# Kernel tuning notes

Hardware: AMD Instinct MI355X
Metric: run time of the kernel (lower is better)

Reference implementation:

```python
import jax, jax.numpy as jnp
import numpy as np

WS, SS, NH = 7, 3, 16  # window_size, shift_size, num_heads


def _rel_pos_index(ws):
    coords = np.stack(np.meshgrid(np.arange(ws), np.arange(ws), indexing='ij'))  # (2, ws, ws)
    cf = coords.reshape(2, -1)                       # (2, N)
    rel = (cf[:, :, None] - cf[:, None, :]).transpose(1, 2, 0).copy()  # (N, N, 2)
    rel[:, :, 0] += ws - 1
    rel[:, :, 1] += ws - 1
    rel[:, :, 0] *= 2 * ws - 1
    return rel.sum(-1)                               # (N, N) int indices into bias table


def _attn_mask(Hp, Wp, ws, ss):
    img = np.zeros((Hp, Wp))
    slices = (slice(0, -ws), slice(-ws, -ss), slice(-ss, None))
    cnt = 0
    for h in slices:
        for w in slices:
            img[h, w] = cnt
            cnt += 1
    mw = img.reshape(Hp // ws, ws, Wp // ws, ws).transpose(0, 2, 1, 3).reshape(-1, ws * ws)  # (nW, N)
    am = mw[:, None, :] - mw[:, :, None]             # (nW, N, N)
    return np.where(am != 0, -100.0, 0.0).astype(np.float32)


def setup_inputs() -> dict:
    key = jax.random.key(0)
    k1, k2, k3, k4 = jax.random.split(key, 4)
    B, H, W, C = 16, 56, 56, 512
    return {
        'q_out': jax.random.normal(k1, (B, H, W, C), dtype=jnp.float32),
        'k_out': jax.random.normal(k2, (B, H, W, C), dtype=jnp.float32),
        'v_out': jax.random.normal(k3, (B, H, W, C), dtype=jnp.float32),
        'bias_table': 0.02 * jax.random.normal(k4, ((2 * WS - 1) ** 2, NH), dtype=jnp.float32),
        'C': C, 'H': H, 'W': W,
        'x_low_padding_h': 0, 'x_low_padding_w': 0,
    }


def reference(q_out, k_out, v_out, bias_table, C, H, W, x_low_padding_h, x_low_padding_w):
    ws, ss, nh = WS, SS, NH
    Hp, Wp = H + x_low_padding_h, W + x_low_padding_w
    B = q_out.shape[0]
    hd = C // nh
    scale = hd ** (-0.5)
    N = ws * ws

    def part(x):  # (B,Hp,Wp,C) -> (B*nW, N, C)
        x = x.reshape(B, Hp // ws, ws, Wp // ws, ws, C).transpose(0, 1, 3, 2, 4, 5)
        return x.reshape(-1, N, C)

    # cyclic shift
    sq = jnp.roll(q_out, (-ss, -ss), axis=(1, 2))
    sk = jnp.roll(k_out, (-ss, -ss), axis=(1, 2))
    sv = jnp.roll(v_out, (-ss, -ss), axis=(1, 2))

    qw, kw, vw = part(sq), part(sk), part(sv)
    B_ = qw.shape[0]
    q = qw.reshape(B_, N, nh, hd).transpose(0, 2, 1, 3) * scale  # (B_, nh, N, hd)
    k = kw.reshape(B_, N, nh, hd).transpose(0, 2, 1, 3)
    v = vw.reshape(B_, N, nh, hd).transpose(0, 2, 1, 3)

    attn = jnp.einsum('bhnd,bhmd->bhnm', q, k)  # (B_, nh, N, N)

    # relative position bias
    rpi = _rel_pos_index(ws)
    bias = bias_table[rpi.reshape(-1)].reshape(N, N, nh).transpose(2, 0, 1)  # (nh, N, N)
    attn = attn + bias[None]

    # shift mask
    am = jnp.asarray(_attn_mask(Hp, Wp, ws, ss), dtype=attn.dtype)  # (nW, N, N)
    nW = am.shape[0]
    attn = attn.reshape(B_ // nW, nW, nh, N, N) + am[None, :, None]
    attn = jax.nn.softmax(attn.reshape(B_, nh, N, N), axis=-1)

    xw = jnp.einsum('bhnm,bhmd->bhnd', attn, v).transpose(0, 2, 1, 3).reshape(B_, N, C)

    # window reverse + reverse shift
    x = xw.reshape(B, Hp // ws, Wp // ws, ws, ws, C).transpose(0, 1, 3, 2, 4, 5).reshape(B, Hp, Wp, C)
    return jnp.roll(x, (ss, ss), axis=(1, 2))
```

## Files before the change

kernel.cpp:

```cpp
#include <hip/hip_runtime.h>
#include <stdint.h>


constexpr int WSZ  = 7;
constexpr int NTOK = 49;
constexpr int NH_  = 16;
constexpr int HD_  = 32;
constexpr int SP   = 56;
constexpr int CH   = 512;
constexpr float LOG2E = 1.4426950408889634f;

typedef float    f32x4 __attribute__((ext_vector_type(4)));
typedef short    s16x8 __attribute__((ext_vector_type(8)));
typedef _Float16 f16x4 __attribute__((ext_vector_type(4)));

union FragU { uint32_t w[4]; s16x8 v; };

__device__ __forceinline__ uint32_t bf16_hibits(float x) {
    uint32_t u = __float_as_uint(x);
    u += 0x7fffu + ((u >> 16) & 1u);
    return u & 0xffff0000u;
}
__device__ __forceinline__ uint32_t pk_bf16(float a, float b) {
    return (bf16_hibits(a) >> 16) | bf16_hibits(b);
}

__global__ __launch_bounds__(256)
void build_bm(const float* __restrict__ bias, _Float16* __restrict__ bm)
{
    const int blk = blockIdx.x;
    const int h = blk >> 2, cls = blk & 3;
    for (int idx = threadIdx.x; idx < 4096; idx += 256) {
        const int q = idx >> 6, m = idx & 63;
        float val;
        if (q >= NTOK || m >= NTOK) {
            val = -1000.0f;
        } else {
            const int iq = q / 7, jq = q % 7, im = m / 7, jm = m % 7;
            const int rpi = (iq - im + 6) * 13 + (jq - jm + 6);
            const float bv = bias[rpi * NH_ + h];
            const int rq = ((cls & 2) ? (iq < 4 ? 3 : 6) : 0)
                         + ((cls & 1) ? (jq < 4 ? 1 : 2) : 0);
            const int rm = ((cls & 2) ? (im < 4 ? 3 : 6) : 0)
                         + ((cls & 1) ? (jm < 4 ? 1 : 2) : 0);
            const float mask = (rq != rm) ? -100.0f : 0.0f;
            val = (bv + mask) * LOG2E;
        }
        bm[blk * 4096 + idx] = (_Float16)val;
    }
}

struct Raw {
    float4 q[4][2];
    float4 k[4][2];
    float  v[2][2][8];
};
struct Frag {
    s16x8 Qh[4], Kh[4], Vb[2][2];
};

__device__ __forceinline__ int make_off(int wh, int lane) {
    const int h  = wh & 15;
    const int w  = wh >> 4;
    const int wc = w & 7, wr = (w >> 3) & 7, b = w >> 6;
    const int t  = lane < NTOK ? lane : NTOK - 1;
    const int it = t / 7, jt = t - 7 * it;
    int sr = wr * 7 + it + 3; if (sr >= SP) sr -= SP;
    int sc = wc * 7 + jt + 3; if (sc >= SP) sc -= SP;
    return ((b * SP + sr) * SP + sc) * CH + h * HD_;
}
__device__ __forceinline__ int cls_of(int wh) {
    const int w = wh >> 4;
    return ((((w >> 3) & 7) == 7) ? 2 : 0) | (((w & 7) == 7) ? 1 : 0);
}

__device__ __forceinline__ void issue_qkv(const float* __restrict__ qg,
                                          const float* __restrict__ kg,
                                          const float* __restrict__ vg,
                                          int off, int l16, int g, Raw& r,
                                          int (&oQK)[4]) {
#pragma unroll
    for (int tt = 0; tt < 4; ++tt) oQK[tt] = __shfl(off, 16 * tt + l16);
    int oV[16];
#pragma unroll
    for (int mc = 0; mc < 2; ++mc)
#pragma unroll
        for (int e = 0; e < 8; ++e) oV[8 * mc + e] = __shfl(off, 32 * mc + 8 * g + e);
#pragma unroll
    for (int tt = 0; tt < 4; ++tt) {
        const float* qp = qg + oQK[tt] + 8 * g;
        const float* kp = kg + oQK[tt] + 8 * g;
        r.q[tt][0] = *(const float4*)qp;  r.q[tt][1] = *(const float4*)(qp + 4);
        r.k[tt][0] = *(const float4*)kp;  r.k[tt][1] = *(const float4*)(kp + 4);
    }
#pragma unroll
    for (int mc = 0; mc < 2; ++mc)
#pragma unroll
        for (int dh = 0; dh < 2; ++dh)
#pragma unroll
            for (int e = 0; e < 8; ++e)
                r.v[mc][dh][e] = vg[oV[8 * mc + e] + 16 * dh + l16];
}

__device__ __forceinline__ void convertQKV(const Raw& r, float qs, Frag& f) {
#pragma unroll
    for (int tt = 0; tt < 4; ++tt) {
        FragU qh, kh;
        qh.w[0] = pk_bf16(r.q[tt][0].x * qs, r.q[tt][0].y * qs);
        qh.w[1] = pk_bf16(r.q[tt][0].z * qs, r.q[tt][0].w * qs);
        qh.w[2] = pk_bf16(r.q[tt][1].x * qs, r.q[tt][1].y * qs);
        qh.w[3] = pk_bf16(r.q[tt][1].z * qs, r.q[tt][1].w * qs);
        kh.w[0] = pk_bf16(r.k[tt][0].x, r.k[tt][0].y);
        kh.w[1] = pk_bf16(r.k[tt][0].z, r.k[tt][0].w);
        kh.w[2] = pk_bf16(r.k[tt][1].x, r.k[tt][1].y);
        kh.w[3] = pk_bf16(r.k[tt][1].z, r.k[tt][1].w);
        f.Qh[tt] = qh.v; f.Kh[tt] = kh.v;
    }
#pragma unroll
    for (int mc = 0; mc < 2; ++mc)
#pragma unroll
        for (int dh = 0; dh < 2; ++dh) {
            FragU fu;
#pragma unroll
            for (int wd = 0; wd < 4; ++wd)
                fu.w[wd] = pk_bf16(r.v[mc][dh][2 * wd], r.v[mc][dh][2 * wd + 1]);
            f.Vb[mc][dh] = fu.v;
        }
}

__device__ __forceinline__ void load_bm(const _Float16* __restrict__ bmh,
                                        int l16, int g, f16x4 (&bmr)[4][4]) {
#pragma unroll
    for (int tq = 0; tq < 4; ++tq)
#pragma unroll
        for (int tk = 0; tk < 4; ++tk)
            bmr[tq][tk] = *(const f16x4*)(bmh + (16 * tq + l16) * 64 + 16 * tk + 4 * g);
}

__device__ __forceinline__ void do_math(const Frag& f, const f16x4 (&bmr)[4][4],
                                        const int (&oQK)[4], int lane, int g, int l16,
                                        float* __restrict__ outg) {
    uint32_t u0[4][4], u1[4][4];
    float inv[4];
#pragma unroll
    for (int tq = 0; tq < 4; ++tq) {
        float dsum = 0.f;
#pragma unroll
        for (int tk = 0; tk < 4; ++tk) {
            f32x4 a;
            a[0] = (float)bmr[tq][tk][0] - 23.f;
            a[1] = (float)bmr[tq][tk][1] - 23.f;
            a[2] = (float)bmr[tq][tk][2] - 23.f;
            a[3] = (float)bmr[tq][tk][3] - 23.f;
            a = __builtin_amdgcn_mfma_f32_16x16x32_bf16(f.Kh[tk], f.Qh[tq], a, 0, 0, 0);
            float e0 = __builtin_amdgcn_exp2f(a[0]);
            float e1 = __builtin_amdgcn_exp2f(a[1]);
            float e2 = __builtin_amdgcn_exp2f(a[2]);
            float e3 = __builtin_amdgcn_exp2f(a[3]);
            dsum += (e0 + e1) + (e2 + e3);
            u0[tq][tk] = pk_bf16(e0, e1);
            u1[tq][tk] = pk_bf16(e2, e3);
        }
        dsum += __shfl_xor(dsum, 16);
        dsum += __shfl_xor(dsum, 32);
        inv[tq] = 1.0f / (dsum + 1e-30f);
    }

    const int srcb = 32 * (g & 1) + l16;
    const bool hiG = (lane >= 32);
    s16x8 PA[4][2];
#pragma unroll
    for (int tq = 0; tq < 4; ++tq)
#pragma unroll
        for (int mc = 0; mc < 2; ++mc) {
            FragU fu;
#pragma unroll
            for (int wd = 0; wd < 4; ++wd) {
                const int sl = srcb + 16 * (wd >> 1);
                uint32_t A, B;
                if (wd & 1) {
                    A = __shfl(u1[tq][2 * mc],     sl);
                    B = __shfl(u1[tq][2 * mc + 1], sl);
                } else {
                    A = __shfl(u0[tq][2 * mc],     sl);
                    B = __shfl(u0[tq][2 * mc + 1], sl);
                }
                fu.w[wd] = hiG ? B : A;
            }
            PA[tq][mc] = fu.v;
        }

#pragma unroll
    for (int tq = 0; tq < 4; ++tq) {
        const float iv = inv[tq];
        const bool ok = (tq < 3) || (l16 == 0);
#pragma unroll
        for (int dh = 0; dh < 2; ++dh) {
            f32x4 a = {0.f, 0.f, 0.f, 0.f};
            a = __builtin_amdgcn_mfma_f32_16x16x32_bf16(f.Vb[0][dh], PA[tq][0], a, 0, 0, 0);
            a = __builtin_amdgcn_mfma_f32_16x16x32_bf16(f.Vb[1][dh], PA[tq][1], a, 0, 0, 0);
            if (ok) {
                float4 st;
                st.x = a[0] * iv; st.y = a[1] * iv;
                st.z = a[2] * iv; st.w = a[3] * iv;
                *(float4*)(outg + oQK[tq] + 16 * dh + 4 * g) = st;
            }
        }
    }
}

__global__ __launch_bounds__(256, 2)
void swin_pipe_kernel(const float* __restrict__ qg,
                      const float* __restrict__ kg,
                      const float* __restrict__ vg,
                      const _Float16* __restrict__ bm,
                      float* __restrict__ outg)
{
    const int wave = threadIdx.x >> 6;
    const int gw   = blockIdx.x * 4 + wave;
    const int lane = threadIdx.x & 63;
    const int g    = lane >> 4;
    const int l16  = lane & 15;
    const float qs = 0.17677669529663687f * LOG2E;

    const int h = gw & 15;
    const _Float16* bmhead = bm + (size_t)h * 4 * 4096;

    Raw A, B;
    Frag f;
    f16x4 bmr[4][4];
    int oA[4], oB[4];

    const int wh0 = gw;
    const int off0 = make_off(wh0, lane);
    issue_qkv(qg, kg, vg, off0, l16, g, A, oA);

    convertQKV(A, qs, f);
    load_bm(bmhead + cls_of(wh0) * 4096, l16, g, bmr);
    const int wh1 = gw + 4096;
    const int off1 = make_off(wh1, lane);
    issue_qkv(qg, kg, vg, off1, l16, g, B, oB);
    __builtin_amdgcn_sched_barrier(0);
    do_math(f, bmr, oA, lane, g, l16, outg);

    convertQKV(B, qs, f);
    load_bm(bmhead + cls_of(wh1) * 4096, l16, g, bmr);
    const int wh2 = gw + 8192;
    const int off2 = make_off(wh2, lane);
    issue_qkv(qg, kg, vg, off2, l16, g, A, oA);
    __builtin_amdgcn_sched_barrier(0);
    do_math(f, bmr, oB, lane, g, l16, outg);

    convertQKV(A, qs, f);
    load_bm(bmhead + cls_of(wh2) * 4096, l16, g, bmr);
    const int wh3 = gw + 12288;
    const int off3 = make_off(wh3, lane);
    issue_qkv(qg, kg, vg, off3, l16, g, B, oB);
    __builtin_amdgcn_sched_barrier(0);
    do_math(f, bmr, oA, lane, g, l16, outg);

    convertQKV(B, qs, f);
    load_bm(bmhead + cls_of(wh3) * 4096, l16, g, bmr);
    __builtin_amdgcn_sched_barrier(0);
    do_math(f, bmr, oB, lane, g, l16, outg);
}

__global__ __launch_bounds__(256)
void swin_block_scalar(const float* __restrict__ qg,
                       const float* __restrict__ kg,
                       const float* __restrict__ vg,
                       const float* __restrict__ bias,
                       float* __restrict__ outg)
{
    const int wave = __builtin_amdgcn_readfirstlane(threadIdx.x >> 6);
    const int wh   = blockIdx.x * 4 + wave;
    const int h    = wh & (NH_ - 1);
    const int w    = wh >> 4;
    const int wc   = w & 7;
    const int wr   = (w >> 3) & 7;
    const int b    = w >> 6;

    const int lane = threadIdx.x & 63;
    const int rr   = lane < NTOK ? lane : NTOK - 1;
    const int i    = rr / WSZ;
    const int j    = rr - i * WSZ;

    const int hp = wr * WSZ + i;
    const int wp = wc * WSZ + j;
    int sr = hp + 3; if (sr >= SP) sr -= SP;
    int sc = wp + 3; if (sc >= SP) sc -= SP;
    const int rowoff = ((b * SP + sr) * SP + sc) * CH + h * HD_;
    const int reg_r = (hp < 49 ? 0 : (hp < 53 ? 3 : 6))
                    + (wp < 49 ? 0 : (wp < 53 ? 1 : 2));
    const float qscale = 0.17677669529663687f * LOG2E;

    float qr[HD_];
    {
        const float4* qp = reinterpret_cast<const float4*>(qg + rowoff);
#pragma unroll
        for (int tt = 0; tt < HD_ / 4; ++tt) {
            float4 x = qp[tt];
            qr[4*tt+0] = x.x * qscale; qr[4*tt+1] = x.y * qscale;
            qr[4*tt+2] = x.z * qscale; qr[4*tt+3] = x.w * qscale;
        }
    }
    const int biaslane = (i * 13 + j) * 16 + h;
    float o[HD_];
#pragma unroll
    for (int d = 0; d < HD_; ++d) o[d] = 0.f;
    float denom = 0.f;
    const float* kb = kg + b * SP * SP * CH + h * HD_;
    const float* vb = vg + b * SP * SP * CH + h * HD_;

    for (int ic = 0; ic < WSZ; ++ic) {
        const int hpc = wr * WSZ + ic;
        int src_r = hpc + 3; if (src_r >= SP) src_r -= SP;
        const int regh_c = (hpc < 49 ? 0 : (hpc < 53 ? 3 : 6));
        const float* krow0 = kb + src_r * SP * CH;
        const float* vrow0 = vb + src_r * SP * CH;
        float e[WSZ];
#pragma unroll
        for (int u = 0; u < WSZ; ++u) {
            const int wpc = wc * WSZ + u;
            int src_c = wpc + 3; if (src_c >= SP) src_c -= SP;
            const int reg_c = regh_c + (wpc < 49 ? 0 : (wpc < 53 ? 1 : 2));
            const float* krow = krow0 + src_c * CH;
            const float bv = bias[biaslane + ((6 - ic) * 13 + (6 - u)) * 16];
            float s0 = fmaf(bv, LOG2E, (reg_r != reg_c) ? -167.26950408889634f : -23.0f);
            float s1 = 0.f, s2 = 0.f, s3 = 0.f;
#pragma unroll
            for (int d = 0; d < HD_; d += 4) {
                s0 = fmaf(qr[d+0], krow[d+0], s0);
                s1 = fmaf(qr[d+1], krow[d+1], s1);
                s2 = fmaf(qr[d+2], krow[d+2], s2);
                s3 = fmaf(qr[d+3], krow[d+3], s3);
            }
            e[u] = exp2f((s0 + s1) + (s2 + s3));
            denom += e[u];
        }
#pragma unroll
        for (int u = 0; u < WSZ; ++u) {
            const int wpc = wc * WSZ + u;
            int src_c = wpc + 3; if (src_c >= SP) src_c -= SP;
            const float* vrow = vrow0 + src_c * CH;
            const float ev = e[u];
#pragma unroll
            for (int d = 0; d < HD_; ++d) o[d] = fmaf(ev, vrow[d], o[d]);
        }
    }
    const float invd = 1.0f / denom;
    if (lane < NTOK) {
        float4* op = reinterpret_cast<float4*>(outg + rowoff);
#pragma unroll
        for (int tt = 0; tt < HD_ / 4; ++tt) {
            float4 x;
            x.x = o[4*tt+0] * invd; x.y = o[4*tt+1] * invd;
            x.z = o[4*tt+2] * invd; x.w = o[4*tt+3] * invd;
            op[tt] = x;
        }
    }
}

extern "C" void kernel_launch(void* const* d_in, const int* in_sizes, int n_in,
                              void* d_out, int out_size, void* d_ws, size_t ws_size,
                              hipStream_t stream) {
    const float* q    = (const float*)d_in[0];
    const float* k    = (const float*)d_in[1];
    const float* v    = (const float*)d_in[2];
    const float* bias = (const float*)d_in[3];
    float* out        = (float*)d_out;

    const int B   = in_sizes[0] / (SP * SP * CH);
    const int nwh = B * (SP / WSZ) * (SP / WSZ) * NH_;

    const size_t bm_bytes = (size_t)NH_ * 4 * 4096 * sizeof(_Float16);
    if (ws_size >= bm_bytes) {
        _Float16* bm = (_Float16*)d_ws;
        hipLaunchKernelGGL(build_bm, dim3(NH_ * 4), dim3(256), 0, stream, bias, bm);
        hipLaunchKernelGGL(swin_pipe_kernel, dim3(nwh / 16), dim3(256), 0, stream,
                           q, k, v, bm, out);
    } else {
        hipLaunchKernelGGL(swin_block_scalar, dim3(nwh / 4), dim3(256), 0, stream,
                           q, k, v, bias, out);
    }
}
```

Before: 111.3 us.

## Stream K through LDS via global_load_lds and shorten per-wave pipeline depth

K tiles are now loaded straight into a per-wave LDS slot with global_load_lds instead of into registers, which frees VGPRs. Launch bounds rise from 2 to 3 blocks per CU and each wave handles 2 windows instead of 4, with twice as many blocks. The aim is more waves in flight to hide memory latency. In exchange, each wave overlaps loads with compute over fewer windows, adds explicit vmcnt/lgkmcnt waits, and reuses one LDS slot, so the first window's K must be fully read out of LDS before the second load overwrites it.

```diff
diff --git a/kernel.cpp b/kernel.cpp
--- a/kernel.cpp
+++ b/kernel.cpp
@@ -10,6 +10,9 @@
 constexpr int CH   = 512;
 constexpr float LOG2E = 1.4426950408889634f;
 
+constexpr int SLOT_BYTES = 8192;
+constexpr size_t LDS_BYTES = 4 * SLOT_BYTES;
+
 typedef float    f32x4 __attribute__((ext_vector_type(4)));
 typedef short    s16x8 __attribute__((ext_vector_type(8)));
 typedef _Float16 f16x4 __attribute__((ext_vector_type(4)));
@@ -23,6 +26,13 @@
 }
 __device__ __forceinline__ uint32_t pk_bf16(float a, float b) {
     return (bf16_hibits(a) >> 16) | bf16_hibits(b);
+}
+
+__device__ __forceinline__ void glds16(const float* g, void* l) {
+    __builtin_amdgcn_global_load_lds(
+        (const __attribute__((address_space(1))) uint32_t*)g,
+        (__attribute__((address_space(3))) uint32_t*)l,
+        16, 0, 0);
 }
 
 __global__ __launch_bounds__(256)
@@ -50,14 +60,8 @@
     }
 }
 
-struct Raw {
-    float4 q[4][2];
-    float4 k[4][2];
-    float  v[2][2][8];
-};
-struct Frag {
-    s16x8 Qh[4], Kh[4], Vb[2][2];
-};
+struct QV { float4 q[4][2]; float v[2][2][8]; };
+struct Frag { s16x8 Qh[4], Kh[4], Vb[2][2]; };
 
 __device__ __forceinline__ int make_off(int wh, int lane) {
     const int h  = wh & 15;
@@ -74,11 +78,21 @@
     return ((((w >> 3) & 7) == 7) ? 2 : 0) | (((w & 7) == 7) ? 1 : 0);
 }
 
-__device__ __forceinline__ void issue_qkv(const float* __restrict__ qg,
-                                          const float* __restrict__ kg,
-                                          const float* __restrict__ vg,
-                                          int off, int l16, int g, Raw& r,
-                                          int (&oQK)[4]) {
+__device__ __forceinline__ void glds_K(const float* __restrict__ kg,
+                                       int off, int l16, int g, char* slot) {
+#pragma unroll
+    for (int tt = 0; tt < 4; ++tt) {
+        const int o = __shfl(off, 16 * tt + l16);
+        const float* kp = kg + o + 8 * g;
+        glds16(kp,     slot + (tt * 2 + 0) * 1024);
+        glds16(kp + 4, slot + (tt * 2 + 1) * 1024);
+    }
+}
+
+__device__ __forceinline__ void issue_qv(const float* __restrict__ qg,
+                                         const float* __restrict__ vg,
+                                         int off, int l16, int g, QV& r,
+                                         int (&oQK)[4]) {
 #pragma unroll
     for (int tt = 0; tt < 4; ++tt) oQK[tt] = __shfl(off, 16 * tt + l16);
     int oV[16];
@@ -89,9 +103,7 @@
 #pragma unroll
     for (int tt = 0; tt < 4; ++tt) {
         const float* qp = qg + oQK[tt] + 8 * g;
-        const float* kp = kg + oQK[tt] + 8 * g;
         r.q[tt][0] = *(const float4*)qp;  r.q[tt][1] = *(const float4*)(qp + 4);
-        r.k[tt][0] = *(const float4*)kp;  r.k[tt][1] = *(const float4*)(kp + 4);
     }
 #pragma unroll
     for (int mc = 0; mc < 2; ++mc)
@@ -102,18 +114,21 @@
                 r.v[mc][dh][e] = vg[oV[8 * mc + e] + 16 * dh + l16];
 }
 
-__device__ __forceinline__ void convertQKV(const Raw& r, float qs, Frag& f) {
+__device__ __forceinline__ void convert_all(const char* slot, const QV& r,
+                                            float qs, int lane, Frag& f) {
 #pragma unroll
     for (int tt = 0; tt < 4; ++tt) {
+        const float4 k0 = *(const float4*)(slot + (tt * 2 + 0) * 1024 + lane * 16);
+        const float4 k1 = *(const float4*)(slot + (tt * 2 + 1) * 1024 + lane * 16);
         FragU qh, kh;
         qh.w[0] = pk_bf16(r.q[tt][0].x * qs, r.q[tt][0].y * qs);
         qh.w[1] = pk_bf16(r.q[tt][0].z * qs, r.q[tt][0].w * qs);
         qh.w[2] = pk_bf16(r.q[tt][1].x * qs, r.q[tt][1].y * qs);
         qh.w[3] = pk_bf16(r.q[tt][1].z * qs, r.q[tt][1].w * qs);
-        kh.w[0] = pk_bf16(r.k[tt][0].x, r.k[tt][0].y);
-        kh.w[1] = pk_bf16(r.k[tt][0].z, r.k[tt][0].w);
-        kh.w[2] = pk_bf16(r.k[tt][1].x, r.k[tt][1].y);
-        kh.w[3] = pk_bf16(r.k[tt][1].z, r.k[tt][1].w);
+        kh.w[0] = pk_bf16(k0.x, k0.y);
+        kh.w[1] = pk_bf16(k0.z, k0.w);
+        kh.w[2] = pk_bf16(k1.x, k1.y);
+        kh.w[3] = pk_bf16(k1.z, k1.w);
         f.Qh[tt] = qh.v; f.Kh[tt] = kh.v;
     }
 #pragma unroll
@@ -209,14 +224,25 @@
     }
 }
 
-__global__ __launch_bounds__(256, 2)
-void swin_pipe_kernel(const float* __restrict__ qg,
-                      const float* __restrict__ kg,
-                      const float* __restrict__ vg,
-                      const _Float16* __restrict__ bm,
-                      float* __restrict__ outg)
+__device__ __forceinline__ void wait_vmem() {
+    asm volatile("s_waitcnt vmcnt(0)" ::: "memory");
+    __builtin_amdgcn_sched_barrier(0);
+}
+__device__ __forceinline__ void drain_lds() {
+    asm volatile("s_waitcnt lgkmcnt(0)" ::: "memory");
+    __builtin_amdgcn_sched_barrier(0);
+}
+
+__global__ __launch_bounds__(256, 3)
+void swin_d2_kernel(const float* __restrict__ qg,
+                    const float* __restrict__ kg,
+                    const float* __restrict__ vg,
+                    const _Float16* __restrict__ bm,
+                    float* __restrict__ outg)
 {
+    extern __shared__ char smem[];
     const int wave = threadIdx.x >> 6;
+    char* slot = smem + wave * SLOT_BYTES;
     const int gw   = blockIdx.x * 4 + wave;
     const int lane = threadIdx.x & 63;
     const int g    = lane >> 4;
@@ -226,43 +252,31 @@
     const int h = gw & 15;
     const _Float16* bmhead = bm + (size_t)h * 4 * 4096;
 
-    Raw A, B;
+    const int wh0 = gw, wh1 = gw + 8192;
+    QV r0, r1;
     Frag f;
     f16x4 bmr[4][4];
-    int oA[4], oB[4];
-
-    const int wh0 = gw;
+    int oQK0[4], oQK1[4];
+
     const int off0 = make_off(wh0, lane);
-    issue_qkv(qg, kg, vg, off0, l16, g, A, oA);
-
-    convertQKV(A, qs, f);
+    glds_K(kg, off0, l16, g, slot);
+    issue_qv(qg, vg, off0, l16, g, r0, oQK0);
+
+    wait_vmem();
+    convert_all(slot, r0, qs, lane, f);
+    drain_lds();
+    const int off1 = make_off(wh1, lane);
+    glds_K(kg, off1, l16, g, slot);
+    issue_qv(qg, vg, off1, l16, g, r1, oQK1);
     load_bm(bmhead + cls_of(wh0) * 4096, l16, g, bmr);
-    const int wh1 = gw + 4096;
-    const int off1 = make_off(wh1, lane);
-    issue_qkv(qg, kg, vg, off1, l16, g, B, oB);
     __builtin_amdgcn_sched_barrier(0);
-    do_math(f, bmr, oA, lane, g, l16, outg);
-
-    convertQKV(B, qs, f);
+    do_math(f, bmr, oQK0, lane, g, l16, outg);
+
+    wait_vmem();
+    convert_all(slot, r1, qs, lane, f);
     load_bm(bmhead + cls_of(wh1) * 4096, l16, g, bmr);
-    const int wh2 = gw + 8192;
-    const int off2 = make_off(wh2, lane);
-    issue_qkv(qg, kg, vg, off2, l16, g, A, oA);
     __builtin_amdgcn_sched_barrier(0);
-    do_math(f, bmr, oB, lane, g, l16, outg);
-
-    convertQKV(A, qs, f);
-    load_bm(bmhead + cls_of(wh2) * 4096, l16, g, bmr);
-    const int wh3 = gw + 12288;
-    const int off3 = make_off(wh3, lane);
-    issue_qkv(qg, kg, vg, off3, l16, g, B, oB);
-    __builtin_amdgcn_sched_barrier(0);
-    do_math(f, bmr, oA, lane, g, l16, outg);
-
-    convertQKV(B, qs, f);
-    load_bm(bmhead + cls_of(wh3) * 4096, l16, g, bmr);
-    __builtin_amdgcn_sched_barrier(0);
-    do_math(f, bmr, oB, lane, g, l16, outg);
+    do_math(f, bmr, oQK1, lane, g, l16, outg);
 }
 
 __global__ __launch_bounds__(256)
@@ -377,8 +391,8 @@
     if (ws_size >= bm_bytes) {
         _Float16* bm = (_Float16*)d_ws;
         hipLaunchKernelGGL(build_bm, dim3(NH_ * 4), dim3(256), 0, stream, bias, bm);
-        hipLaunchKernelGGL(swin_pipe_kernel, dim3(nwh / 16), dim3(256), 0, stream,
-                           q, k, v, bm, out);
+        hipLaunchKernelGGL(swin_d2_kernel, dim3(nwh / 8), dim3(256), LDS_BYTES,
+                           stream, q, k, v, bm, out);
     } else {
         hipLaunchKernelGGL(swin_block_scalar, dim3(nwh / 4), dim3(256), 0, stream,
                            q, k, v, bias, out);
```

Result: slower. 133.5 us (+20.0%).
